# Optimization experiments

Measured on AMD Instinct MI355X. Metric: run time of the kernel, lower is better.

## Reference

```python
import jax, jax.numpy as jnp
import numpy as np

DIM = 128      # d_model (C)
DEPTH = 8
D_INNER = 2 * DIM      # expand=2
D_STATE = 16
D_CONV = 4
DT_RANK = (DIM + 15) // 16  # ceil(d_model/16) = 8
EPS = 1e-6
B_SZ, H_SZ, W_SZ = 2, 64, 64


def setup_inputs() -> dict:
    key = jax.random.key(0)
    ks = jax.random.split(key, 8)
    s = 0.02
    f32 = jnp.float32
    inp = {
        "x": jax.random.normal(ks[0], (B_SZ, DIM, H_SZ, W_SZ), f32),
        "in_proj_w": (jax.random.normal(ks[1], (DEPTH, 2 * D_INNER, DIM), f32) * s),
        "conv_w": (jax.random.normal(ks[2], (DEPTH, D_INNER, D_CONV), f32) * s),
        "conv_b": jnp.zeros((DEPTH, D_INNER), f32),
        "x_proj_w": (jax.random.normal(ks[3], (DEPTH, DT_RANK + 2 * D_STATE, D_INNER), f32) * s),
        "dt_proj_w": (jax.random.normal(ks[4], (DEPTH, D_INNER, DT_RANK), f32) * s),
        "dt_proj_b": jax.random.uniform(ks[5], (DEPTH, D_INNER), f32, -4.0, -2.0),
        "A_log": jnp.tile(jnp.log(jnp.arange(1.0, D_STATE + 1.0, dtype=f32))[None, None, :], (DEPTH, D_INNER, 1)),
        "D_skip": jnp.ones((DEPTH, D_INNER), f32),
        "out_proj_w": (jax.random.normal(ks[6], (DEPTH, DIM, D_INNER), f32) * s),
        "rms_w": jnp.ones((DIM,), f32),
    }
    return inp


def _selective_scan(u, delta, A, Bm, Cm, D_skip):
    # u, delta: [B,L,Dn]; A: [Dn,N]; Bm, Cm: [B,L,N]; D_skip: [Dn]
    dA = jnp.exp(delta[..., None] * A)                      # [B,L,Dn,N]
    dBu = (delta * u)[..., None] * Bm[:, :, None, :]        # [B,L,Dn,N]
    def comb(c1, c2):
        a1, b1 = c1
        a2, b2 = c2
        return a1 * a2, a2 * b1 + b2
    _, h = jax.lax.associative_scan(comb, (dA, dBu), axis=1)  # h: [B,L,Dn,N]
    y = jnp.einsum('bldn,bln->bld', h, Cm) + u * D_skip
    return y


def _mamba_layer(x, in_w, cw, cb, xp_w, dtw, dtb, A_log, D_skip, out_w):
    # x: [B,L,D]
    xz = jnp.einsum('bld,ed->ble', x, in_w)                 # [B,L,2*Dn]
    xin, z = jnp.split(xz, 2, axis=-1)
    # causal depthwise conv1d, kernel D_CONV, left-pad D_CONV-1
    lhs = jnp.transpose(xin, (0, 2, 1))                     # [B,Dn,L]
    rhs = cw[:, None, :]                                    # [Dn,1,K]
    xc = jax.lax.conv_general_dilated(
        lhs, rhs, window_strides=(1,), padding=[(D_CONV - 1, 0)],
        dimension_numbers=('NCH', 'OIH', 'NCH'), feature_group_count=D_INNER)
    xc = xc + cb[None, :, None]
    xc = jax.nn.silu(jnp.transpose(xc, (0, 2, 1)))          # [B,L,Dn]
    x_dbl = jnp.einsum('bld,ed->ble', xc, xp_w)             # [B,L,dt_rank+2N]
    dt, Bm, Cm = jnp.split(x_dbl, [DT_RANK, DT_RANK + D_STATE], axis=-1)
    delta = jax.nn.softplus(jnp.einsum('blr,dr->bld', dt, dtw) + dtb)
    A = -jnp.exp(A_log)                                     # [Dn,N]
    y = _selective_scan(xc, delta, A, Bm, Cm, D_skip)       # [B,L,Dn]
    y = y * jax.nn.silu(z)
    return jnp.einsum('bld,od->blo', y, out_w)              # [B,L,D]


def reference(x, in_proj_w, conv_w, conv_b, x_proj_w, dt_proj_w, dt_proj_b,
              A_log, D_skip, out_proj_w, rms_w):
    B, C, H, W = x.shape
    h = jnp.transpose(x.reshape(B, C, H * W), (0, 2, 1))    # [B,L,C]
    for i in range(DEPTH):
        h = _mamba_layer(h, in_proj_w[i], conv_w[i], conv_b[i], x_proj_w[i],
                         dt_proj_w[i], dt_proj_b[i], A_log[i], D_skip[i],
                         out_proj_w[i])
    # RMSNorm over channel dim
    h = h * jax.lax.rsqrt(jnp.mean(h * h, axis=-1, keepdims=True) + EPS) * rms_w
    return jnp.transpose(h.reshape(B, H, W, C), (0, 3, 1, 2))
```

## Files before the change

### kernel.cpp

```cpp
#include <hip/hip_runtime.h>
#include <math.h>

#define B_SZ   2
#define L_SEQ  4096
#define DIMC   128
#define DI     256
#define DST    16
#define DTR    8
#define NXP    40
#define NXPP   48
#define NLAYER 8
#define NCH    256
#define CS     (L_SEQ / NCH)
#define LOG2E  1.4426950408889634f
#define LN2    0.6931471805599453f
#define PSA    264

typedef __attribute__((ext_vector_type(8))) unsigned short u16x8;
typedef __attribute__((ext_vector_type(4))) float f32x4;

__device__ __forceinline__ float fexp2(float x){ float r; asm("v_exp_f32 %0, %1" : "=v"(r) : "v"(x)); return r; }
__device__ __forceinline__ float flog2(float x){ float r; asm("v_log_f32 %0, %1" : "=v"(r) : "v"(x)); return r; }
__device__ __forceinline__ float frcp (float x){ float r; asm("v_rcp_f32 %0, %1" : "=v"(r) : "v"(x)); return r; }

__device__ __forceinline__ float silu_f(float x) {
    return x * frcp(1.f + fexp2(-x * LOG2E));
}
__device__ __forceinline__ float softplus_f(float x) {
    float t = fexp2(-fabsf(x) * LOG2E);
    return fmaxf(x, 0.f) + flog2(1.f + t) * LN2;
}
__device__ __forceinline__ void splitf(float x, unsigned short& h, unsigned short& l) {
    unsigned bx = __builtin_bit_cast(unsigned, x);
    h = (unsigned short)(bx >> 16);
    float fh = __builtin_bit_cast(float, bx & 0xffff0000u);
    float r = x - fh;
    l = (unsigned short)(__builtin_bit_cast(unsigned, r) >> 16);
}
__device__ __forceinline__ float bf2f(unsigned short u) {
    return __builtin_bit_cast(float, (unsigned)u << 16);
}

__global__ void split_arr(const float* __restrict__ s, unsigned short* __restrict__ hi,
                          unsigned short* __restrict__ lo, int n) {
    int i = (blockIdx.x * 256 + threadIdx.x) * 4;
    if (i >= n) return;
    #pragma unroll
    for (int j = 0; j < 4; ++j) {
        unsigned short h, l;
        splitf(s[i + j], h, l);
        hi[i + j] = h; lo[i + j] = l;
    }
}

__global__ void split_xpw(const float* __restrict__ s, unsigned short* __restrict__ hi,
                          unsigned short* __restrict__ lo) {
    int i = blockIdx.x * 256 + threadIdx.x;
    int layer = i / (NXPP * DI);
    int rem   = i % (NXPP * DI);
    int c = rem / DI, k = rem % DI;
    unsigned short h = 0, l = 0;
    if (c < NXP) splitf(s[((size_t)layer * NXP + c) * DI + k], h, l);
    hi[i] = h; lo[i] = l;
}

__global__ void transpose_in(const float* __restrict__ x, unsigned short* __restrict__ hh,
                             unsigned short* __restrict__ hl) {
    __shared__ float tl[32][33];
    const int b  = blockIdx.x;
    const int c0 = blockIdx.y * 32;
    const int l0 = blockIdx.z * 32;
    const int tx = threadIdx.x;
    const int ty = threadIdx.y;
    #pragma unroll
    for (int r = 0; r < 4; ++r) {
        int c = c0 + ty + r * 8;
        tl[ty + r * 8][tx] = x[((size_t)b * DIMC + c) * L_SEQ + l0 + tx];
    }
    __syncthreads();
    #pragma unroll
    for (int r = 0; r < 4; ++r) {
        int l = l0 + ty + r * 8;
        float v = tl[tx][ty + r * 8];
        size_t o = ((size_t)b * L_SEQ + l) * DIMC + c0 + tx;
        unsigned short h16, l16; splitf(v, h16, l16);
        hh[o] = h16; hl[o] = l16;
    }
}

template<int BM, int BN>
__global__ __launch_bounds__(256) void gemm_sp(
    const unsigned short* __restrict__ Ahg, const unsigned short* __restrict__ Alg,
    const unsigned short* __restrict__ Whg, const unsigned short* __restrict__ Wlg,
    float* __restrict__ C, int M, int N, int K) {
    constexpr int PS = 40;
    __shared__ unsigned short lds[(BM + BN) * 2 * PS];
    unsigned short* LAh = lds;
    unsigned short* LAl = LAh + BM * PS;
    unsigned short* LBh = LAl + BM * PS;
    unsigned short* LBl = LBh + BN * PS;
    const int t = threadIdx.x;
    const int w = t >> 6, l = t & 63;
    const int wr = w >> 1, wc = w & 1;
    const int lr = l & 15, lq = l >> 4;
    constexpr int MF = BM / 32, NF = BN / 32;
    const int bm = blockIdx.x * BM, bn = blockIdx.y * BN;
    f32x4 acc[MF][NF];
    const f32x4 z4 = {0.f, 0.f, 0.f, 0.f};
    #pragma unroll
    for (int m = 0; m < MF; ++m)
        #pragma unroll
        for (int n = 0; n < NF; ++n) acc[m][n] = z4;

    for (int k0 = 0; k0 < K; k0 += 32) {
        if (k0) __syncthreads();
        #pragma unroll
        for (int s = 0; s < BM * 4 / 256; ++s) {
            int task = t + s * 256;
            int r = task >> 2, g = task & 3;
            size_t go = (size_t)(bm + r) * K + k0 + g * 8;
            *(u16x8*)&LAh[r * PS + g * 8] = *(const u16x8*)&Ahg[go];
            *(u16x8*)&LAl[r * PS + g * 8] = *(const u16x8*)&Alg[go];
        }
        #pragma unroll
        for (int s = 0; s < BN * 4 / 256; ++s) {
            int task = t + s * 256;
            int r = task >> 2, g = task & 3;
            size_t go = (size_t)(bn + r) * K + k0 + g * 8;
            *(u16x8*)&LBh[r * PS + g * 8] = *(const u16x8*)&Whg[go];
            *(u16x8*)&LBl[r * PS + g * 8] = *(const u16x8*)&Wlg[go];
        }
        __syncthreads();
        u16x8 ah[MF], al[MF], bh[NF], bl[NF];
        #pragma unroll
        for (int m = 0; m < MF; ++m) {
            int rr = wr * (BM / 2) + m * 16 + lr;
            ah[m] = *(u16x8*)&LAh[rr * PS + lq * 8];
            al[m] = *(u16x8*)&LAl[rr * PS + lq * 8];
        }
        #pragma unroll
        for (int n = 0; n < NF; ++n) {
            int rr = wc * (BN / 2) + n * 16 + lr;
            bh[n] = *(u16x8*)&LBh[rr * PS + lq * 8];
            bl[n] = *(u16x8*)&LBl[rr * PS + lq * 8];
        }
        #pragma unroll
        for (int m = 0; m < MF; ++m)
            #pragma unroll
            for (int n = 0; n < NF; ++n) {
                asm("v_mfma_f32_16x16x32_bf16 %0, %1, %2, %0" : "+v"(acc[m][n]) : "v"(ah[m]), "v"(bh[n]));
                asm("v_mfma_f32_16x16x32_bf16 %0, %1, %2, %0" : "+v"(acc[m][n]) : "v"(ah[m]), "v"(bl[n]));
                asm("v_mfma_f32_16x16x32_bf16 %0, %1, %2, %0" : "+v"(acc[m][n]) : "v"(al[m]), "v"(bh[n]));
            }
    }
    #pragma unroll
    for (int m = 0; m < MF; ++m)
        #pragma unroll
        for (int n = 0; n < NF; ++n) {
            int col = bn + wc * (BN / 2) + n * 16 + lr;
            #pragma unroll
            for (int r = 0; r < 4; ++r) {
                int row = bm + wr * (BM / 2) + m * 16 + lq * 4 + r;
                C[(size_t)row * N + col] = acc[m][n][r];
            }
        }
}

__global__ __launch_bounds__(256) void fused_mid(
    const float* __restrict__ xz,
    const unsigned short* __restrict__ xpwh, const unsigned short* __restrict__ xpwl,
    const float* __restrict__ dtw, const float* __restrict__ dtb,
    const float* __restrict__ cw, const float* __restrict__ cb,
    const float* __restrict__ A_log,
    float* __restrict__ xdbl, float* __restrict__ paO, float* __restrict__ hO) {
    const int ch = blockIdx.x & (NCH - 1);
    const int d  = threadIdx.x;
    const size_t r0 = (size_t)(blockIdx.x >> 8) * L_SEQ + ch * CS;
    __shared__ unsigned short aS[2][CS][PSA];
    __shared__ float P[4][CS][49];
    __shared__ float xdblS[CS][41];

    {
        const float w0 = cw[d * 4 + 0], w1 = cw[d * 4 + 1];
        const float w2 = cw[d * 4 + 2], w3 = cw[d * 4 + 3];
        const float bz = cb[d];
        float p0 = 0.f, p1 = 0.f, p2 = 0.f;
        if (ch > 0) {
            p0 = xz[(r0 - 3) * 512 + d];
            p1 = xz[(r0 - 2) * 512 + d];
            p2 = xz[(r0 - 1) * 512 + d];
        }
        #pragma unroll 4
        for (int i = 0; i < CS; ++i) {
            float cur = xz[(r0 + i) * 512 + d];
            float v = silu_f(fmaf(w3, cur, fmaf(w2, p2, fmaf(w1, p1, fmaf(w0, p0, bz)))));
            unsigned short h16, l16; splitf(v, h16, l16);
            aS[0][i][d] = h16; aS[1][i][d] = l16;
            p0 = p1; p1 = p2; p2 = cur;
        }
    }
    __syncthreads();

    const int w = threadIdx.x >> 6, l = threadIdx.x & 63;
    const int lr = l & 15, lq = l >> 4;
    {
        f32x4 acc[3];
        const f32x4 z4 = {0.f, 0.f, 0.f, 0.f};
        #pragma unroll
        for (int n = 0; n < 3; ++n) acc[n] = z4;
        #pragma unroll
        for (int ks = 0; ks < 2; ++ks) {
            const int kk = w * 64 + ks * 32 + lq * 8;
            u16x8 ah, al, bh[3], bl[3];
            ah = *(const u16x8*)&aS[0][lr][kk];
            al = *(const u16x8*)&aS[1][lr][kk];
            #pragma unroll
            for (int n = 0; n < 3; ++n) {
                const int c = n * 16 + lr;
                bh[n] = *(const u16x8*)&xpwh[c * DI + kk];
                bl[n] = *(const u16x8*)&xpwl[c * DI + kk];
            }
            #pragma unroll
            for (int n = 0; n < 3; ++n) {
                asm("v_mfma_f32_16x16x32_bf16 %0, %1, %2, %0" : "+v"(acc[n]) : "v"(ah), "v"(bh[n]));
                asm("v_mfma_f32_16x16x32_bf16 %0, %1, %2, %0" : "+v"(acc[n]) : "v"(ah), "v"(bl[n]));
                asm("v_mfma_f32_16x16x32_bf16 %0, %1, %2, %0" : "+v"(acc[n]) : "v"(al), "v"(bh[n]));
            }
        }
        #pragma unroll
        for (int n = 0; n < 3; ++n)
            #pragma unroll
            for (int r = 0; r < 4; ++r)
                P[w][lq * 4 + r][n * 16 + lr] = acc[n][r];
    }
    __syncthreads();
    {
        const int i = threadIdx.x >> 4;
        const int cb0 = threadIdx.x & 15;
        for (int c = cb0; c < NXP; c += 16) {
            float s = P[0][i][c] + P[1][i][c] + P[2][i][c] + P[3][i][c];
            xdblS[i][c] = s;
            xdbl[(r0 + i) * NXP + c] = s;
        }
    }
    __syncthreads();

    float wt[DTR];
    #pragma unroll
    for (int r = 0; r < DTR; ++r) wt[r] = dtw[d * DTR + r];
    const float bt = dtb[d];
    float Af[DST], h[DST], pa[DST];
    #pragma unroll
    for (int n = 0; n < DST; ++n) {
        Af[n] = -expf(A_log[d * DST + n]) * LOG2E;
        h[n] = 0.f; pa[n] = 1.f;
    }
    #pragma unroll 4
    for (int i = 0; i < CS; ++i) {
        float s = bt;
        #pragma unroll
        for (int r = 0; r < DTR; ++r) s = fmaf(xdblS[i][r], wt[r], s);
        const float dl = softplus_f(s);
        const float u = bf2f(aS[0][i][d]) + bf2f(aS[1][i][d]);
        const float du = dl * u;
        #pragma unroll
        for (int n = 0; n < DST; ++n) {
            const float dA = fexp2(dl * Af[n]);
            pa[n] *= dA;
            h[n] = fmaf(dA, h[n], du * xdblS[i][DTR + n]);
        }
    }
    const size_t o = ((size_t)blockIdx.x * DI + d) * DST;
    #pragma unroll
    for (int n = 0; n < DST; ++n) { paO[o + n] = pa[n]; hO[o + n] = h[n]; }
}

__global__ void scan_combine(float* __restrict__ paO, const float* __restrict__ hO) {
    const int t  = blockIdx.x * 256 + threadIdx.x;
    const int b  = t / (DI * DST);
    const int dn = t % (DI * DST);
    float run = 0.f;
    for (int ch0 = 0; ch0 < NCH; ch0 += 8) {
        float pav[8], hv[8];
        #pragma unroll
        for (int j = 0; j < 8; ++j) {
            size_t o = ((size_t)(b * NCH + ch0 + j)) * DI * DST + dn;
            pav[j] = paO[o]; hv[j] = hO[o];
        }
        #pragma unroll
        for (int j = 0; j < 8; ++j) {
            size_t o = ((size_t)(b * NCH + ch0 + j)) * DI * DST + dn;
            paO[o] = run;
            run = fmaf(pav[j], run, hv[j]);
        }
    }
}

__global__ __launch_bounds__(256) void fused_out(
    const float* __restrict__ xz, const float* __restrict__ xdbl,
    const unsigned short* __restrict__ owh, const unsigned short* __restrict__ owl,
    const float* __restrict__ dtw, const float* __restrict__ dtb,
    const float* __restrict__ cw, const float* __restrict__ cb,
    const float* __restrict__ A_log, const float* __restrict__ D_skip,
    const float* __restrict__ hinit,
    unsigned short* __restrict__ hh, unsigned short* __restrict__ hl) {
    const int ch = blockIdx.x & (NCH - 1);
    const int d  = threadIdx.x;
    const size_t r0 = (size_t)(blockIdx.x >> 8) * L_SEQ + ch * CS;
    __shared__ unsigned short yS[2][CS][PSA];
    __shared__ float xdblS[CS][41];

    {
        const float* src = xdbl + r0 * NXP;
        for (int idx = threadIdx.x; idx < CS * NXP; idx += 256)
            xdblS[idx / NXP][idx % NXP] = src[idx];
    }
    float wt[DTR];
    #pragma unroll
    for (int r = 0; r < DTR; ++r) wt[r] = dtw[d * DTR + r];
    const float bt = dtb[d];
    const float Dd = D_skip[d];
    const float w0 = cw[d * 4 + 0], w1 = cw[d * 4 + 1];
    const float w2 = cw[d * 4 + 2], w3 = cw[d * 4 + 3];
    const float bz = cb[d];
    float Af[DST], h[DST];
    const size_t o = ((size_t)blockIdx.x * DI + d) * DST;
    #pragma unroll
    for (int n = 0; n < DST; ++n) {
        Af[n] = -expf(A_log[d * DST + n]) * LOG2E;
        h[n] = hinit[o + n];
    }
    float p0 = 0.f, p1 = 0.f, p2 = 0.f;
    if (ch > 0) {
        p0 = xz[(r0 - 3) * 512 + d];
        p1 = xz[(r0 - 2) * 512 + d];
        p2 = xz[(r0 - 1) * 512 + d];
    }
    __syncthreads();

    #pragma unroll 4
    for (int i = 0; i < CS; ++i) {
        const float cur = xz[(r0 + i) * 512 + d];
        const float zv  = xz[(r0 + i) * 512 + DI + d];
        const float u = silu_f(fmaf(w3, cur, fmaf(w2, p2, fmaf(w1, p1, fmaf(w0, p0, bz)))));
        p0 = p1; p1 = p2; p2 = cur;
        float s = bt;
        #pragma unroll
        for (int r = 0; r < DTR; ++r) s = fmaf(xdblS[i][r], wt[r], s);
        const float dl = softplus_f(s);
        const float du = dl * u;
        float acc = 0.f;
        #pragma unroll
        for (int n = 0; n < DST; ++n) {
            const float dA = fexp2(dl * Af[n]);
            h[n] = fmaf(dA, h[n], du * xdblS[i][DTR + n]);
            acc = fmaf(h[n], xdblS[i][DTR + DST + n], acc);
        }
        const float y = (acc + u * Dd) * silu_f(zv);
        unsigned short h16, l16; splitf(y, h16, l16);
        yS[0][i][d] = h16; yS[1][i][d] = l16;
    }
    __syncthreads();

    const int w = threadIdx.x >> 6, l = threadIdx.x & 63;
    const int lr = l & 15, lq = l >> 4;
    f32x4 acc[2];
    const f32x4 z4 = {0.f, 0.f, 0.f, 0.f};
    #pragma unroll
    for (int n = 0; n < 2; ++n) acc[n] = z4;
    #pragma unroll
    for (int ks = 0; ks < 8; ++ks) {
        const int kk = ks * 32 + lq * 8;
        u16x8 ah, al, bh[2], bl[2];
        ah = *(const u16x8*)&yS[0][lr][kk];
        al = *(const u16x8*)&yS[1][lr][kk];
        #pragma unroll
        for (int n = 0; n < 2; ++n) {
            const int c = w * 32 + n * 16 + lr;
            bh[n] = *(const u16x8*)&owh[c * DI + kk];
            bl[n] = *(const u16x8*)&owl[c * DI + kk];
        }
        #pragma unroll
        for (int n = 0; n < 2; ++n) {
            asm("v_mfma_f32_16x16x32_bf16 %0, %1, %2, %0" : "+v"(acc[n]) : "v"(ah), "v"(bh[n]));
            asm("v_mfma_f32_16x16x32_bf16 %0, %1, %2, %0" : "+v"(acc[n]) : "v"(ah), "v"(bl[n]));
            asm("v_mfma_f32_16x16x32_bf16 %0, %1, %2, %0" : "+v"(acc[n]) : "v"(al), "v"(bh[n]));
        }
    }
    #pragma unroll
    for (int n = 0; n < 2; ++n) {
        const int col = w * 32 + n * 16 + lr;
        #pragma unroll
        for (int r = 0; r < 4; ++r) {
            const size_t row = r0 + lq * 4 + r;
            unsigned short h16, l16; splitf(acc[n][r], h16, l16);
            hh[row * DIMC + col] = h16;
            hl[row * DIMC + col] = l16;
        }
    }
}

__global__ void rms_out(const unsigned short* __restrict__ hh, const unsigned short* __restrict__ hl,
                        const float* __restrict__ rw, float* __restrict__ out) {
    __shared__ float tile[64][129];
    __shared__ float rinv[64];
    const int blk = blockIdx.x;
    const int b = blk / (L_SEQ / 64);
    const int l0 = (blk % (L_SEQ / 64)) * 64;
    const int t = threadIdx.x;
    for (int k = 0; k < 32; ++k) {
        int idx = k * 256 + t;
        int l = idx >> 7, cc = idx & 127;
        size_t o = ((size_t)b * L_SEQ + l0 + l) * DIMC + cc;
        tile[l][cc] = bf2f(hh[o]) + bf2f(hl[o]);
    }
    __syncthreads();
    if (t < 64) {
        float s = 0.f;
        for (int cc = 0; cc < DIMC; ++cc) { float v = tile[t][cc]; s += v * v; }
        rinv[t] = rsqrtf(s / DIMC + 1e-6f);
    }
    __syncthreads();
    for (int k = 0; k < 32; ++k) {
        int odx = k * 256 + t;
        int cc = odx >> 6, li = odx & 63;
        out[((size_t)b * DIMC + cc) * L_SEQ + l0 + li] = tile[li][cc] * rinv[li] * rw[cc];
    }
}

extern "C" void kernel_launch(void* const* d_in, const int* in_sizes, int n_in,
                              void* d_out, int out_size, void* d_ws, size_t ws_size,
                              hipStream_t stream) {
    const float* x      = (const float*)d_in[0];
    const float* in_w   = (const float*)d_in[1];
    const float* conv_w = (const float*)d_in[2];
    const float* conv_b = (const float*)d_in[3];
    const float* xp_w   = (const float*)d_in[4];
    const float* dt_w   = (const float*)d_in[5];
    const float* dt_b   = (const float*)d_in[6];
    const float* A_log  = (const float*)d_in[7];
    const float* D_skip = (const float*)d_in[8];
    const float* out_w  = (const float*)d_in[9];
    const float* rms_w  = (const float*)d_in[10];
    float* out = (float*)d_out;

    const int M = B_SZ * L_SEQ;
    char* p = (char*)d_ws;
    auto alloc = [&](size_t bytes) -> void* {
        void* r = (void*)p; p += (bytes + 255) & ~(size_t)255; return r;
    };
    float* xz   = (float*)alloc((size_t)M * 512 * 4);
    float* xdbl = (float*)alloc((size_t)M * NXP * 4);
    float* paB  = (float*)alloc((size_t)B_SZ * NCH * DI * DST * 4);
    float* hB   = (float*)alloc((size_t)B_SZ * NCH * DI * DST * 4);
    unsigned short* hh0 = (unsigned short*)alloc((size_t)M * DIMC * 2);
    unsigned short* hl0 = (unsigned short*)alloc((size_t)M * DIMC * 2);
    unsigned short* hh1 = (unsigned short*)alloc((size_t)M * DIMC * 2);
    unsigned short* hl1 = (unsigned short*)alloc((size_t)M * DIMC * 2);
    unsigned short* iwh = (unsigned short*)alloc((size_t)NLAYER * 512 * 128 * 2);
    unsigned short* iwl = (unsigned short*)alloc((size_t)NLAYER * 512 * 128 * 2);
    unsigned short* xpwh = (unsigned short*)alloc((size_t)NLAYER * NXPP * DI * 2);
    unsigned short* xpwl = (unsigned short*)alloc((size_t)NLAYER * NXPP * DI * 2);
    unsigned short* owh = (unsigned short*)alloc((size_t)NLAYER * DIMC * DI * 2);
    unsigned short* owl = (unsigned short*)alloc((size_t)NLAYER * DIMC * DI * 2);

    split_arr<<<(NLAYER * 512 * 128) / 1024, 256, 0, stream>>>(in_w, iwh, iwl, NLAYER * 512 * 128);
    split_xpw<<<(NLAYER * NXPP * DI) / 256, 256, 0, stream>>>(xp_w, xpwh, xpwl);
    split_arr<<<(NLAYER * DIMC * DI) / 1024, 256, 0, stream>>>(out_w, owh, owl, NLAYER * DIMC * DI);

    transpose_in<<<dim3(B_SZ, DIMC / 32, L_SEQ / 32), dim3(32, 8), 0, stream>>>(x, hh0, hl0);

    unsigned short *hhin = hh0, *hlin = hl0, *hhout = hh1, *hlout = hl1;
    for (int layer = 0; layer < NLAYER; ++layer) {
        const float* cw  = conv_w + (size_t)layer * DI * 4;
        const float* cb  = conv_b + (size_t)layer * DI;
        const float* dtw = dt_w   + (size_t)layer * DI * DTR;
        const float* dtb = dt_b   + (size_t)layer * DI;
        const float* al  = A_log  + (size_t)layer * DI * DST;
        const float* ds  = D_skip + (size_t)layer * DI;
        const size_t iwo = (size_t)layer * 512 * 128;
        const size_t xpo = (size_t)layer * NXPP * DI;
        const size_t owo = (size_t)layer * DIMC * DI;

        gemm_sp<64, 128><<<dim3(M / 64, 4), 256, 0, stream>>>(
            hhin, hlin, iwh + iwo, iwl + iwo, xz, M, 512, 128);
        fused_mid<<<B_SZ * NCH, 256, 0, stream>>>(
            xz, xpwh + xpo, xpwl + xpo, dtw, dtb, cw, cb, al, xdbl, paB, hB);
        scan_combine<<<(B_SZ * DI * DST) / 256, 256, 0, stream>>>(paB, hB);
        fused_out<<<B_SZ * NCH, 256, 0, stream>>>(
            xz, xdbl, owh + owo, owl + owo, dtw, dtb, cw, cb, al, ds, paB,
            hhout, hlout);

        unsigned short* ts;
        ts = hhin; hhin = hhout; hhout = ts;
        ts = hlin; hlin = hlout; hlout = ts;
    }

    rms_out<<<B_SZ * (L_SEQ / 64), 256, 0, stream>>>(hhin, hlin, rms_w, out);
}
```

Measured before the change: 577.3 us.

## Halve scan chunk size, cache conv output, precompute A, merge prep kernels

Doubles the number of sequence chunks from 256 to 512 (8 rows each) to launch more blocks for the mid and out kernels. The MFMA tiles are zero-padded to 16 rows and only the valid half is stored. The conv+SiLU output is now written as a bf16 hi/lo pair in fused_mid and reread in fused_out instead of being recomputed. -exp(A_log) is precomputed once and the three weight-split kernels are merged into one prep kernel. The input-projection GEMM tile also changes to 64x64. The trade-offs are half-wasted MFMA work, extra global traffic for u, and a longer sequential scan_combine over twice as many chunks.

```diff
diff --git a/kernel.cpp b/kernel.cpp
--- a/kernel.cpp
+++ b/kernel.cpp
@@ -10,7 +10,7 @@
 #define NXP    40
 #define NXPP   48
 #define NLAYER 8
-#define NCH    256
+#define NCH    512
 #define CS     (L_SEQ / NCH)
 #define LOG2E  1.4426950408889634f
 #define LN2    0.6931471805599453f
@@ -41,27 +41,28 @@
     return __builtin_bit_cast(float, (unsigned)u << 16);
 }
 
-__global__ void split_arr(const float* __restrict__ s, unsigned short* __restrict__ hi,
-                          unsigned short* __restrict__ lo, int n) {
-    int i = (blockIdx.x * 256 + threadIdx.x) * 4;
-    if (i >= n) return;
-    #pragma unroll
-    for (int j = 0; j < 4; ++j) {
-        unsigned short h, l;
-        splitf(s[i + j], h, l);
-        hi[i + j] = h; lo[i + j] = l;
-    }
-}
-
-__global__ void split_xpw(const float* __restrict__ s, unsigned short* __restrict__ hi,
-                          unsigned short* __restrict__ lo) {
-    int i = blockIdx.x * 256 + threadIdx.x;
-    int layer = i / (NXPP * DI);
-    int rem   = i % (NXPP * DI);
-    int c = rem / DI, k = rem % DI;
-    unsigned short h = 0, l = 0;
-    if (c < NXP) splitf(s[((size_t)layer * NXP + c) * DI + k], h, l);
-    hi[i] = h; lo[i] = l;
+#define N_INW  (NLAYER * 512 * 128)
+#define N_XPW  (NLAYER * NXPP * DI)
+#define N_OW   (NLAYER * DIMC * DI)
+#define N_AF   (NLAYER * DI * DST)
+__global__ void prep(const float* __restrict__ in_w, const float* __restrict__ xp_w,
+                     const float* __restrict__ out_w, const float* __restrict__ A_log,
+                     unsigned short* __restrict__ iwh, unsigned short* __restrict__ iwl,
+                     unsigned short* __restrict__ xpwh, unsigned short* __restrict__ xpwl,
+                     unsigned short* __restrict__ owh, unsigned short* __restrict__ owl,
+                     float* __restrict__ Af) {
+    const int i = blockIdx.x * 256 + threadIdx.x;
+    if (i < N_INW) { unsigned short h, l; splitf(in_w[i], h, l); iwh[i] = h; iwl[i] = l; }
+    if (i < N_XPW) {
+        int layer = i / (NXPP * DI);
+        int rem   = i % (NXPP * DI);
+        int c = rem / DI, k = rem % DI;
+        unsigned short h = 0, l = 0;
+        if (c < NXP) splitf(xp_w[((size_t)layer * NXP + c) * DI + k], h, l);
+        xpwh[i] = h; xpwl[i] = l;
+    }
+    if (i < N_OW) { unsigned short h, l; splitf(out_w[i], h, l); owh[i] = h; owl[i] = l; }
+    if (i < N_AF) Af[i] = -expf(A_log[i]) * LOG2E;
 }
 
 __global__ void transpose_in(const float* __restrict__ x, unsigned short* __restrict__ hh,
@@ -171,14 +172,18 @@
     const unsigned short* __restrict__ xpwh, const unsigned short* __restrict__ xpwl,
     const float* __restrict__ dtw, const float* __restrict__ dtb,
     const float* __restrict__ cw, const float* __restrict__ cb,
-    const float* __restrict__ A_log,
-    float* __restrict__ xdbl, float* __restrict__ paO, float* __restrict__ hO) {
+    const float* __restrict__ Af_g,
+    float* __restrict__ xdbl, unsigned short* __restrict__ uh, unsigned short* __restrict__ ul,
+    float* __restrict__ paO, float* __restrict__ hO) {
     const int ch = blockIdx.x & (NCH - 1);
     const int d  = threadIdx.x;
-    const size_t r0 = (size_t)(blockIdx.x >> 8) * L_SEQ + ch * CS;
-    __shared__ unsigned short aS[2][CS][PSA];
+    const size_t r0 = (size_t)(blockIdx.x >> 9) * L_SEQ + ch * CS;
+    __shared__ unsigned short aS[2][16][PSA];
     __shared__ float P[4][CS][49];
     __shared__ float xdblS[CS][41];
+
+    #pragma unroll
+    for (int i = 8; i < 16; ++i) { aS[0][i][d] = 0; aS[1][i][d] = 0; }
 
     {
         const float w0 = cw[d * 4 + 0], w1 = cw[d * 4 + 1];
@@ -190,12 +195,13 @@
             p1 = xz[(r0 - 2) * 512 + d];
             p2 = xz[(r0 - 1) * 512 + d];
         }
-        #pragma unroll 4
+        #pragma unroll
         for (int i = 0; i < CS; ++i) {
             float cur = xz[(r0 + i) * 512 + d];
             float v = silu_f(fmaf(w3, cur, fmaf(w2, p2, fmaf(w1, p1, fmaf(w0, p0, bz)))));
             unsigned short h16, l16; splitf(v, h16, l16);
             aS[0][i][d] = h16; aS[1][i][d] = l16;
+            uh[(r0 + i) * DI + d] = h16; ul[(r0 + i) * DI + d] = l16;
             p0 = p1; p1 = p2; p2 = cur;
         }
     }
@@ -227,20 +233,26 @@
                 asm("v_mfma_f32_16x16x32_bf16 %0, %1, %2, %0" : "+v"(acc[n]) : "v"(al), "v"(bh[n]));
             }
         }
-        #pragma unroll
-        for (int n = 0; n < 3; ++n)
+        if (lq < 2) {
             #pragma unroll
-            for (int r = 0; r < 4; ++r)
-                P[w][lq * 4 + r][n * 16 + lr] = acc[n][r];
+            for (int n = 0; n < 3; ++n)
+                #pragma unroll
+                for (int r = 0; r < 4; ++r)
+                    P[w][lq * 4 + r][n * 16 + lr] = acc[n][r];
+        }
     }
     __syncthreads();
     {
-        const int i = threadIdx.x >> 4;
-        const int cb0 = threadIdx.x & 15;
-        for (int c = cb0; c < NXP; c += 16) {
-            float s = P[0][i][c] + P[1][i][c] + P[2][i][c] + P[3][i][c];
-            xdblS[i][c] = s;
-            xdbl[(r0 + i) * NXP + c] = s;
+        const int i = threadIdx.x >> 5;
+        const int c = threadIdx.x & 31;
+        float s = P[0][i][c] + P[1][i][c] + P[2][i][c] + P[3][i][c];
+        xdblS[i][c] = s;
+        xdbl[(r0 + i) * NXP + c] = s;
+        if (c < 8) {
+            const int c2 = c + 32;
+            float s2 = P[0][i][c2] + P[1][i][c2] + P[2][i][c2] + P[3][i][c2];
+            xdblS[i][c2] = s2;
+            xdbl[(r0 + i) * NXP + c2] = s2;
         }
     }
     __syncthreads();
@@ -252,10 +264,10 @@
     float Af[DST], h[DST], pa[DST];
     #pragma unroll
     for (int n = 0; n < DST; ++n) {
-        Af[n] = -expf(A_log[d * DST + n]) * LOG2E;
+        Af[n] = Af_g[d * DST + n];
         h[n] = 0.f; pa[n] = 1.f;
     }
-    #pragma unroll 4
+    #pragma unroll
     for (int i = 0; i < CS; ++i) {
         float s = bt;
         #pragma unroll
@@ -298,18 +310,20 @@
 
 __global__ __launch_bounds__(256) void fused_out(
     const float* __restrict__ xz, const float* __restrict__ xdbl,
+    const unsigned short* __restrict__ uh, const unsigned short* __restrict__ ul,
     const unsigned short* __restrict__ owh, const unsigned short* __restrict__ owl,
     const float* __restrict__ dtw, const float* __restrict__ dtb,
-    const float* __restrict__ cw, const float* __restrict__ cb,
-    const float* __restrict__ A_log, const float* __restrict__ D_skip,
+    const float* __restrict__ Af_g, const float* __restrict__ D_skip,
     const float* __restrict__ hinit,
     unsigned short* __restrict__ hh, unsigned short* __restrict__ hl) {
     const int ch = blockIdx.x & (NCH - 1);
     const int d  = threadIdx.x;
-    const size_t r0 = (size_t)(blockIdx.x >> 8) * L_SEQ + ch * CS;
-    __shared__ unsigned short yS[2][CS][PSA];
+    const size_t r0 = (size_t)(blockIdx.x >> 9) * L_SEQ + ch * CS;
+    __shared__ unsigned short yS[2][16][PSA];
     __shared__ float xdblS[CS][41];
 
+    #pragma unroll
+    for (int i = 8; i < 16; ++i) { yS[0][i][d] = 0; yS[1][i][d] = 0; }
     {
         const float* src = xdbl + r0 * NXP;
         for (int idx = threadIdx.x; idx < CS * NXP; idx += 256)
@@ -320,30 +334,19 @@
     for (int r = 0; r < DTR; ++r) wt[r] = dtw[d * DTR + r];
     const float bt = dtb[d];
     const float Dd = D_skip[d];
-    const float w0 = cw[d * 4 + 0], w1 = cw[d * 4 + 1];
-    const float w2 = cw[d * 4 + 2], w3 = cw[d * 4 + 3];
-    const float bz = cb[d];
     float Af[DST], h[DST];
     const size_t o = ((size_t)blockIdx.x * DI + d) * DST;
     #pragma unroll
     for (int n = 0; n < DST; ++n) {
-        Af[n] = -expf(A_log[d * DST + n]) * LOG2E;
+        Af[n] = Af_g[d * DST + n];
         h[n] = hinit[o + n];
     }
-    float p0 = 0.f, p1 = 0.f, p2 = 0.f;
-    if (ch > 0) {
-        p0 = xz[(r0 - 3) * 512 + d];
-        p1 = xz[(r0 - 2) * 512 + d];
-        p2 = xz[(r0 - 1) * 512 + d];
-    }
-    __syncthreads();
-
-    #pragma unroll 4
+    __syncthreads();
+
+    #pragma unroll
     for (int i = 0; i < CS; ++i) {
-        const float cur = xz[(r0 + i) * 512 + d];
-        const float zv  = xz[(r0 + i) * 512 + DI + d];
-        const float u = silu_f(fmaf(w3, cur, fmaf(w2, p2, fmaf(w1, p1, fmaf(w0, p0, bz)))));
-        p0 = p1; p1 = p2; p2 = cur;
+        const float u  = bf2f(uh[(r0 + i) * DI + d]) + bf2f(ul[(r0 + i) * DI + d]);
+        const float zv = xz[(r0 + i) * 512 + DI + d];
         float s = bt;
         #pragma unroll
         for (int r = 0; r < DTR; ++r) s = fmaf(xdblS[i][r], wt[r], s);
@@ -387,15 +390,17 @@
             asm("v_mfma_f32_16x16x32_bf16 %0, %1, %2, %0" : "+v"(acc[n]) : "v"(al), "v"(bh[n]));
         }
     }
-    #pragma unroll
-    for (int n = 0; n < 2; ++n) {
-        const int col = w * 32 + n * 16 + lr;
-        #pragma unroll
-        for (int r = 0; r < 4; ++r) {
-            const size_t row = r0 + lq * 4 + r;
-            unsigned short h16, l16; splitf(acc[n][r], h16, l16);
-            hh[row * DIMC + col] = h16;
-            hl[row * DIMC + col] = l16;
+    if (lq < 2) {
+        #pragma unroll
+        for (int n = 0; n < 2; ++n) {
+            const int col = w * 32 + n * 16 + lr;
+            #pragma unroll
+            for (int r = 0; r < 4; ++r) {
+                const size_t row = r0 + lq * 4 + r;
+                unsigned short h16, l16; splitf(acc[n][r], h16, l16);
+                hh[row * DIMC + col] = h16;
+                hl[row * DIMC + col] = l16;
+            }
         }
     }
 }
@@ -453,20 +458,22 @@
     float* xdbl = (float*)alloc((size_t)M * NXP * 4);
     float* paB  = (float*)alloc((size_t)B_SZ * NCH * DI * DST * 4);
     float* hB   = (float*)alloc((size_t)B_SZ * NCH * DI * DST * 4);
+    float* AfT  = (float*)alloc((size_t)N_AF * 4);
+    unsigned short* uh  = (unsigned short*)alloc((size_t)M * DI * 2);
+    unsigned short* ul  = (unsigned short*)alloc((size_t)M * DI * 2);
     unsigned short* hh0 = (unsigned short*)alloc((size_t)M * DIMC * 2);
     unsigned short* hl0 = (unsigned short*)alloc((size_t)M * DIMC * 2);
     unsigned short* hh1 = (unsigned short*)alloc((size_t)M * DIMC * 2);
     unsigned short* hl1 = (unsigned short*)alloc((size_t)M * DIMC * 2);
-    unsigned short* iwh = (unsigned short*)alloc((size_t)NLAYER * 512 * 128 * 2);
-    unsigned short* iwl = (unsigned short*)alloc((size_t)NLAYER * 512 * 128 * 2);
-    unsigned short* xpwh = (unsigned short*)alloc((size_t)NLAYER * NXPP * DI * 2);
-    unsigned short* xpwl = (unsigned short*)alloc((size_t)NLAYER * NXPP * DI * 2);
-    unsigned short* owh = (unsigned short*)alloc((size_t)NLAYER * DIMC * DI * 2);
-    unsigned short* owl = (unsigned short*)alloc((size_t)NLAYER * DIMC * DI * 2);
-
-    split_arr<<<(NLAYER * 512 * 128) / 1024, 256, 0, stream>>>(in_w, iwh, iwl, NLAYER * 512 * 128);
-    split_xpw<<<(NLAYER * NXPP * DI) / 256, 256, 0, stream>>>(xp_w, xpwh, xpwl);
-    split_arr<<<(NLAYER * DIMC * DI) / 1024, 256, 0, stream>>>(out_w, owh, owl, NLAYER * DIMC * DI);
+    unsigned short* iwh = (unsigned short*)alloc((size_t)N_INW * 2);
+    unsigned short* iwl = (unsigned short*)alloc((size_t)N_INW * 2);
+    unsigned short* xpwh = (unsigned short*)alloc((size_t)N_XPW * 2);
+    unsigned short* xpwl = (unsigned short*)alloc((size_t)N_XPW * 2);
+    unsigned short* owh = (unsigned short*)alloc((size_t)N_OW * 2);
+    unsigned short* owl = (unsigned short*)alloc((size_t)N_OW * 2);
+
+    prep<<<(N_INW + 255) / 256, 256, 0, stream>>>(
+        in_w, xp_w, out_w, A_log, iwh, iwl, xpwh, xpwl, owh, owl, AfT);
 
     transpose_in<<<dim3(B_SZ, DIMC / 32, L_SEQ / 32), dim3(32, 8), 0, stream>>>(x, hh0, hl0);
 
@@ -476,19 +483,19 @@
         const float* cb  = conv_b + (size_t)layer * DI;
         const float* dtw = dt_w   + (size_t)layer * DI * DTR;
         const float* dtb = dt_b   + (size_t)layer * DI;
-        const float* al  = A_log  + (size_t)layer * DI * DST;
+        const float* af  = AfT    + (size_t)layer * DI * DST;
         const float* ds  = D_skip + (size_t)layer * DI;
         const size_t iwo = (size_t)layer * 512 * 128;
         const size_t xpo = (size_t)layer * NXPP * DI;
         const size_t owo = (size_t)layer * DIMC * DI;
 
-        gemm_sp<64, 128><<<dim3(M / 64, 4), 256, 0, stream>>>(
+        gemm_sp<64, 64><<<dim3(M / 64, 8), 256, 0, stream>>>(
             hhin, hlin, iwh + iwo, iwl + iwo, xz, M, 512, 128);
         fused_mid<<<B_SZ * NCH, 256, 0, stream>>>(
-            xz, xpwh + xpo, xpwl + xpo, dtw, dtb, cw, cb, al, xdbl, paB, hB);
+            xz, xpwh + xpo, xpwl + xpo, dtw, dtb, cw, cb, af, xdbl, uh, ul, paB, hB);
         scan_combine<<<(B_SZ * DI * DST) / 256, 256, 0, stream>>>(paB, hB);
         fused_out<<<B_SZ * NCH, 256, 0, stream>>>(
-            xz, xdbl, owh + owo, owl + owo, dtw, dtb, cw, cb, al, ds, paB,
+            xz, xdbl, uh, ul, owh + owo, owl + owo, dtw, dtb, af, ds, paB,
             hhout, hlout);
 
         unsigned short* ts;
```

Result: slower. 746.8 us (+29.4%).
